# Kernel tuning notes

Measured on AMD Instinct MI355X. Metric: run time of the kernel, lower is better.

## Reference

```python
import jax, jax.numpy as jnp
import numpy as np

# db4 decomposition low-pass filter, pywt coefficient order
DEC_LO = np.array([-0.010597401784997278, 0.032883011666982945,
                   0.030841381835986965, -0.18703481171888114,
                   -0.02798376941698385, 0.6308807679295904,
                   0.7148465705525415, 0.23037781330885523], dtype=np.float32)
LEVEL = 5
B, C, L = 64, 64, 8192


def _qmf_hi(dec_lo):
    # pywt relation: dec_hi[n] = (-1)^(n+1) * dec_lo[F-1-n]
    F = dec_lo.shape[0]
    signs = jnp.where(jnp.arange(F) % 2 == 0, -1.0, 1.0).astype(dec_lo.dtype)
    return signs * dec_lo[::-1]


def _wavedec(x, dec_lo, dec_hi):
    # pywt.dwt(v, w, 'symmetric') == np.convolve(sym_pad(v, F-1), filt, 'valid')[1::2]
    # implemented as a stride-2 cross-correlation with the reversed filter.
    b, c, n = x.shape
    v = x.reshape(b * c, n)
    F = dec_lo.shape[0]
    # kernel: (out_ch=2 [lo, hi], in_ch=1, width=F); reversed => true convolution
    k = jnp.stack([dec_lo[::-1], dec_hi[::-1]])[:, None, :]
    details = []
    for _ in range(LEVEL):
        ext = jnp.pad(v, ((0, 0), (F - 1, F - 1)), mode='symmetric')[:, 1:]
        y = jax.lax.conv_general_dilated(ext[:, None, :], k,
                                         window_strides=(2,), padding='VALID')
        v = y[:, 0, :]           # approximation -> next level input
        details.append(y[:, 1, :])  # detail for this level (finest first)
    approx = v.reshape(b, c, -1)
    # pywt order: [cA_L, cD_L, ..., cD_1] -> coarsest detail first
    det = [d.reshape(b, c, -1) for d in reversed(details)]
    return (approx, *det)


def setup_inputs() -> dict:
    key = jax.random.key(0)
    x = jax.random.normal(key, (B, C, L), dtype=jnp.float32)
    dec_lo = jnp.asarray(DEC_LO)
    dec_hi = _qmf_hi(dec_lo)
    return {"x": x, "dec_lo": dec_lo, "dec_hi": dec_hi}


def reference(x, dec_lo, dec_hi):
    # Returns (cA_L, cD_L, cD_{L-1}, ..., cD_1), matching the torch module's
    # [approx_tensor, detail_tensors] flattened.
    return _wavedec(x, dec_lo, dec_hi)
```

## Files before the change

### kernel.cpp

```cpp
#include <hip/hip_runtime.h>


static constexpr int ROWS = 4096;
static constexpr int N0 = 8192;
static constexpr int L1n = 4099, L2n = 2053, L3n = 1030, L4n = 518, L5n = 262;
static constexpr size_t OFF_D5 = 1073152u;
static constexpr size_t OFF_D4 = 2146304u;
static constexpr size_t OFF_D3 = 4268032u;
static constexpr size_t OFF_D2 = 8486912u;
static constexpr size_t OFF_D1 = 16896000u;

__device__ __forceinline__ float refl_load(const float* __restrict__ s, int idx, int n) {
    int i = (idx < 0) ? (-1 - idx) : ((idx >= n) ? (2 * n - 1 - idx) : idx);
    return s[i];
}

__device__ __forceinline__ void load_win(const float* __restrict__ src, int j,
                                         float* __restrict__ w) {
    const float2* __restrict__ s2 = reinterpret_cast<const float2*>(src) + (4 * j - 3);
#pragma unroll
    for (int t = 0; t < 8; ++t) {
        const float2 v = s2[t];
        w[2 * t] = v.x; w[2 * t + 1] = v.y;
    }
}

__device__ __forceinline__ void compute_store(
    const float* __restrict__ w,
    const float* __restrict__ h, const float* __restrict__ g,
    float* __restrict__ adst, float* __restrict__ ddst, int p0)
{
    float aa[4], dd[4];
#pragma unroll
    for (int r = 0; r < 4; ++r) {
        float a = 0.f, d = 0.f;
#pragma unroll
        for (int q = 0; q < 8; ++q) {
            const float v = w[2 * r + 7 - q];
            a = fmaf(h[q], v, a);
            d = fmaf(g[q], v, d);
        }
        aa[r] = a; dd[r] = d;
    }
#pragma unroll
    for (int r = 0; r < 4; ++r) ddst[p0 + r] = dd[r];
#pragma unroll
    for (int r = 0; r < 4; ++r) adst[p0 + r] = aa[r];
}

__device__ __forceinline__ void edge_group(
    const float* __restrict__ src, int n, int m,
    const float* __restrict__ h, const float* __restrict__ g,
    float* __restrict__ adst, float* __restrict__ ddst, int j)
{
#pragma unroll 4
    for (int r = 0; r < 4; ++r) {
        const int pos = 4 * j + r;
        if (pos >= m) break;
        const int s0 = 2 * pos + 1;
        float a = 0.f, d = 0.f;
#pragma unroll
        for (int q = 0; q < 8; ++q) {
            const float v = refl_load(src, s0 - q, n);
            a = fmaf(h[q], v, a);
            d = fmaf(g[q], v, d);
        }
        ddst[pos] = d;
        adst[pos] = a;
    }
}

__device__ __forceinline__ void dwt_level(
    const float* __restrict__ src, int n, int m,
    const float* __restrict__ h, const float* __restrict__ g,
    float* __restrict__ adst, float* __restrict__ ddst, int tid)
{
    const int G = (m + 3) >> 2;
    const int H = (G + 1) >> 1;
    const int jmax = (n - 10) >> 3;

    for (int j = tid; j < H; j += 256) {
        const int j2 = j + H;
        const bool v2 = (j2 < G);
        const bool i1 = (j >= 1) && (j <= jmax) && (4 * j + 3 < m);
        const bool i2 = v2 && (j2 <= jmax) && (4 * j2 + 3 < m);

        float w1[16], w2[16];
        if (i1) load_win(src, j,  w1);
        if (i2) load_win(src, j2, w2);

        if (i1) compute_store(w1, h, g, adst, ddst, 4 * j);
        else    edge_group(src, n, m, h, g, adst, ddst, j);

        if (i2)      compute_store(w2, h, g, adst, ddst, 4 * j2);
        else if (v2) edge_group(src, n, m, h, g, adst, ddst, j2);
    }
}

__global__ __launch_bounds__(256, 4)
void wavedec5_kernel(const float* __restrict__ x,
                     const float* __restrict__ dlo,
                     const float* __restrict__ dhi,
                     float* __restrict__ out)
{
    __shared__ __align__(16) float bufA[4100];
    __shared__ __align__(16) float bufB[2056];

    const int row = blockIdx.x;
    const int tid = threadIdx.x;

    float h[8], g[8];
#pragma unroll
    for (int i = 0; i < 8; ++i) { h[i] = dlo[i]; g[i] = dhi[i]; }

    const float* __restrict__ xr = x + (size_t)row * N0;

    dwt_level(xr, N0, L1n, h, g, bufA,
              out + OFF_D1 + (size_t)row * L1n, tid);
    __syncthreads();
    dwt_level(bufA, L1n, L2n, h, g, bufB,
              out + OFF_D2 + (size_t)row * L2n, tid);
    __syncthreads();
    dwt_level(bufB, L2n, L3n, h, g, bufA,
              out + OFF_D3 + (size_t)row * L3n, tid);
    __syncthreads();
    dwt_level(bufA, L3n, L4n, h, g, bufB,
              out + OFF_D4 + (size_t)row * L4n, tid);
    __syncthreads();
    dwt_level(bufB, L4n, L5n, h, g,
              out + (size_t)row * L5n,
              out + OFF_D5 + (size_t)row * L5n, tid);
}

extern "C" void kernel_launch(void* const* d_in, const int* in_sizes, int n_in,
                              void* d_out, int out_size, void* d_ws, size_t ws_size,
                              hipStream_t stream) {
    const float* x   = (const float*)d_in[0];
    const float* dlo = (const float*)d_in[1];
    const float* dhi = (const float*)d_in[2];
    float* out = (float*)d_out;
    wavedec5_kernel<<<ROWS, 256, 0, stream>>>(x, dlo, dhi, out);
}
```

Baseline: 62.42 us.

## Process two rows per block with interleaved per-thread work across rows

Each block now handles two signal rows. Every thread computes the same output group for both rows instead of two groups of one row, which doubles the LDS footprint and halves the grid size. The goal is to spread the per-level sync cost and the coarse-level underutilization over more work, and to expose more independent loads per thread. The launch bounds drop the min blocks per CU from 4 to 3. With half as many blocks there is less block-level parallelism, and the higher LDS use per block may lower occupancy.

```diff
diff --git a/kernel.cpp b/kernel.cpp
--- a/kernel.cpp
+++ b/kernel.cpp
@@ -25,29 +25,6 @@
     }
 }
 
-__device__ __forceinline__ void compute_store(
-    const float* __restrict__ w,
-    const float* __restrict__ h, const float* __restrict__ g,
-    float* __restrict__ adst, float* __restrict__ ddst, int p0)
-{
-    float aa[4], dd[4];
-#pragma unroll
-    for (int r = 0; r < 4; ++r) {
-        float a = 0.f, d = 0.f;
-#pragma unroll
-        for (int q = 0; q < 8; ++q) {
-            const float v = w[2 * r + 7 - q];
-            a = fmaf(h[q], v, a);
-            d = fmaf(g[q], v, d);
-        }
-        aa[r] = a; dd[r] = d;
-    }
-#pragma unroll
-    for (int r = 0; r < 4; ++r) ddst[p0 + r] = dd[r];
-#pragma unroll
-    for (int r = 0; r < 4; ++r) adst[p0 + r] = aa[r];
-}
-
 __device__ __forceinline__ void edge_group(
     const float* __restrict__ src, int n, int m,
     const float* __restrict__ h, const float* __restrict__ g,
@@ -70,66 +47,92 @@
     }
 }
 
-__device__ __forceinline__ void dwt_level(
-    const float* __restrict__ src, int n, int m,
+__device__ __forceinline__ void dwt_level2(
+    const float* __restrict__ s0, const float* __restrict__ s1, int n, int m,
     const float* __restrict__ h, const float* __restrict__ g,
-    float* __restrict__ adst, float* __restrict__ ddst, int tid)
+    float* __restrict__ a0, float* __restrict__ a1,
+    float* __restrict__ d0, float* __restrict__ d1, int tid)
 {
     const int G = (m + 3) >> 2;
-    const int H = (G + 1) >> 1;
     const int jmax = (n - 10) >> 3;
 
-    for (int j = tid; j < H; j += 256) {
-        const int j2 = j + H;
-        const bool v2 = (j2 < G);
-        const bool i1 = (j >= 1) && (j <= jmax) && (4 * j + 3 < m);
-        const bool i2 = v2 && (j2 <= jmax) && (4 * j2 + 3 < m);
-
-        float w1[16], w2[16];
-        if (i1) load_win(src, j,  w1);
-        if (i2) load_win(src, j2, w2);
-
-        if (i1) compute_store(w1, h, g, adst, ddst, 4 * j);
-        else    edge_group(src, n, m, h, g, adst, ddst, j);
-
-        if (i2)      compute_store(w2, h, g, adst, ddst, 4 * j2);
-        else if (v2) edge_group(src, n, m, h, g, adst, ddst, j2);
+    for (int j = tid; j < G; j += 256) {
+        const int p0 = 4 * j;
+        if (j >= 1 && j <= jmax && p0 + 3 < m) {
+            float w0[16], w1[16];
+            load_win(s0, j, w0);
+            load_win(s1, j, w1);
+            float aa0[4], dd0[4], aa1[4], dd1[4];
+#pragma unroll
+            for (int r = 0; r < 4; ++r) {
+                float x0 = 0.f, y0 = 0.f, x1 = 0.f, y1 = 0.f;
+#pragma unroll
+                for (int q = 0; q < 8; ++q) {
+                    const float u0 = w0[2 * r + 7 - q];
+                    const float u1 = w1[2 * r + 7 - q];
+                    x0 = fmaf(h[q], u0, x0);
+                    y0 = fmaf(g[q], u0, y0);
+                    x1 = fmaf(h[q], u1, x1);
+                    y1 = fmaf(g[q], u1, y1);
+                }
+                aa0[r] = x0; dd0[r] = y0;
+                aa1[r] = x1; dd1[r] = y1;
+            }
+#pragma unroll
+            for (int r = 0; r < 4; ++r) d0[p0 + r] = dd0[r];
+#pragma unroll
+            for (int r = 0; r < 4; ++r) d1[p0 + r] = dd1[r];
+#pragma unroll
+            for (int r = 0; r < 4; ++r) a0[p0 + r] = aa0[r];
+#pragma unroll
+            for (int r = 0; r < 4; ++r) a1[p0 + r] = aa1[r];
+        } else {
+            edge_group(s0, n, m, h, g, a0, d0, j);
+            edge_group(s1, n, m, h, g, a1, d1, j);
+        }
     }
 }
 
-__global__ __launch_bounds__(256, 4)
+__global__ __launch_bounds__(256, 3)
 void wavedec5_kernel(const float* __restrict__ x,
                      const float* __restrict__ dlo,
                      const float* __restrict__ dhi,
                      float* __restrict__ out)
 {
-    __shared__ __align__(16) float bufA[4100];
-    __shared__ __align__(16) float bufB[2056];
+    __shared__ __align__(16) float bufA[2][4100];
+    __shared__ __align__(16) float bufB[2][2056];
 
-    const int row = blockIdx.x;
-    const int tid = threadIdx.x;
+    const int tid  = threadIdx.x;
+    const int row0 = blockIdx.x << 1;
+    const int row1 = row0 + 1;
 
     float h[8], g[8];
 #pragma unroll
     for (int i = 0; i < 8; ++i) { h[i] = dlo[i]; g[i] = dhi[i]; }
 
-    const float* __restrict__ xr = x + (size_t)row * N0;
+    const float* __restrict__ xr0 = x + (size_t)row0 * N0;
+    const float* __restrict__ xr1 = x + (size_t)row1 * N0;
 
-    dwt_level(xr, N0, L1n, h, g, bufA,
-              out + OFF_D1 + (size_t)row * L1n, tid);
+    dwt_level2(xr0, xr1, N0, L1n, h, g, bufA[0], bufA[1],
+               out + OFF_D1 + (size_t)row0 * L1n,
+               out + OFF_D1 + (size_t)row1 * L1n, tid);
     __syncthreads();
-    dwt_level(bufA, L1n, L2n, h, g, bufB,
-              out + OFF_D2 + (size_t)row * L2n, tid);
+    dwt_level2(bufA[0], bufA[1], L1n, L2n, h, g, bufB[0], bufB[1],
+               out + OFF_D2 + (size_t)row0 * L2n,
+               out + OFF_D2 + (size_t)row1 * L2n, tid);
     __syncthreads();
-    dwt_level(bufB, L2n, L3n, h, g, bufA,
-              out + OFF_D3 + (size_t)row * L3n, tid);
+    dwt_level2(bufB[0], bufB[1], L2n, L3n, h, g, bufA[0], bufA[1],
+               out + OFF_D3 + (size_t)row0 * L3n,
+               out + OFF_D3 + (size_t)row1 * L3n, tid);
     __syncthreads();
-    dwt_level(bufA, L3n, L4n, h, g, bufB,
-              out + OFF_D4 + (size_t)row * L4n, tid);
+    dwt_level2(bufA[0], bufA[1], L3n, L4n, h, g, bufB[0], bufB[1],
+               out + OFF_D4 + (size_t)row0 * L4n,
+               out + OFF_D4 + (size_t)row1 * L4n, tid);
     __syncthreads();
-    dwt_level(bufB, L4n, L5n, h, g,
-              out + (size_t)row * L5n,
-              out + OFF_D5 + (size_t)row * L5n, tid);
+    dwt_level2(bufB[0], bufB[1], L4n, L5n, h, g,
+               out + (size_t)row0 * L5n, out + (size_t)row1 * L5n,
+               out + OFF_D5 + (size_t)row0 * L5n,
+               out + OFF_D5 + (size_t)row1 * L5n, tid);
 }
 
 extern "C" void kernel_launch(void* const* d_in, const int* in_sizes, int n_in,
@@ -139,5 +142,5 @@
     const float* dlo = (const float*)d_in[1];
     const float* dhi = (const float*)d_in[2];
     float* out = (float*)d_out;
-    wavedec5_kernel<<<ROWS, 256, 0, stream>>>(x, dlo, dhi, out);
+    wavedec5_kernel<<<ROWS / 2, 256, 0, stream>>>(x, dlo, dhi, out);
 }
```

Result: slower. 71.83 us (+15.1%).
